# Performance work log

Measured on AMD Instinct MI355X. Metric: run time of the kernel, lower is better.

Reference implementation:

```python
import jax, jax.numpy as jnp
import numpy as np

B, S, D_IN, D_OUT, H = 4, 2048, 1024, 1024, 16
HD = D_OUT // H

def setup_inputs() -> dict:
    key = jax.random.key(0)
    ks = jax.random.split(key, 6)
    s = 1.0 / np.sqrt(D_IN)
    return {
        "x": jax.random.normal(ks[0], (B, S, D_IN), dtype=jnp.float32),
        "Wq": jax.random.uniform(ks[1], (D_IN, D_OUT), jnp.float32, -s, s),
        "Wk": jax.random.uniform(ks[2], (D_IN, D_OUT), jnp.float32, -s, s),
        "Wv": jax.random.uniform(ks[3], (D_IN, D_OUT), jnp.float32, -s, s),
        "Wo": jax.random.uniform(ks[4], (D_OUT, D_OUT), jnp.float32, -s, s),
        "bo": jax.random.uniform(ks[5], (D_OUT,), jnp.float32, -s, s),
    }

def reference(x, Wq, Wk, Wv, Wo, bo):
    b, n, _ = x.shape
    # project and split heads: [b, h, n, hd]
    q = (x @ Wq).reshape(b, n, H, HD).transpose(0, 2, 1, 3)
    k = (x @ Wk).reshape(b, n, H, HD).transpose(0, 2, 1, 3)
    v = (x @ Wv).reshape(b, n, H, HD).transpose(0, 2, 1, 3)
    scores = jnp.einsum("bhqd,bhkd->bhqk", q, k) / np.sqrt(HD).astype(np.float32)
    causal = jnp.tril(jnp.ones((n, n), dtype=bool))
    scores = jnp.where(causal, scores, -jnp.inf)
    attn = jax.nn.softmax(scores, axis=-1)  # dropout p=0.0 -> identity
    ctx = jnp.einsum("bhqk,bhkd->bhqd", attn, v)
    ctx = ctx.transpose(0, 2, 1, 3).reshape(b, n, D_OUT)
    return ctx @ Wo + bo
```

## Files before the change

kernel.cpp:

```cpp
#include <hip/hip_runtime.h>
#include <stdint.h>

#define B_   4
#define S_   2048
#define DI   1024
#define DOUT 1024
#define NHD  16
#define HD   64

typedef __attribute__((ext_vector_type(8))) short short8;
typedef __attribute__((ext_vector_type(4))) float f32x4;
typedef __attribute__((ext_vector_type(16))) float f32x16;

__device__ __forceinline__ unsigned short f32_bf16(float f) {
  union { float f; unsigned u; } v; v.f = f;
  unsigned r = v.u + 0x7FFFu + ((v.u >> 16) & 1u);
  return (unsigned short)(r >> 16);
}

__device__ __forceinline__ unsigned cvt_pk_bf16(float a, float b) {
  unsigned r;
  asm("v_cvt_pk_bf16_f32 %0, %1, %2" : "=v"(r) : "v"(a), "v"(b));
  return r;
}

__device__ __forceinline__ void pl32swap(unsigned &dst, unsigned &src) {
  asm("v_permlane32_swap_b32 %0, %1" : "+v"(dst), "+v"(src));
}

__device__ __forceinline__ float max3f(float a, float b, float c) {
  float d;
  asm("v_max3_f32 %0, %1, %2, %3" : "=v"(d) : "v"(a), "v"(b), "v"(c));
  return d;
}

__device__ __forceinline__ void gl_lds16(const void* g, void* s) {
  __builtin_amdgcn_global_load_lds(
      (const __attribute__((address_space(1))) unsigned int*)g,
      (__attribute__((address_space(3))) unsigned int*)s, 16, 0, 0);
}

#define EXP2(x) __builtin_amdgcn_exp2f(x)

__global__ __launch_bounds__(256) void cvt_kernel(const float* __restrict__ src,
                                                  unsigned short* __restrict__ dst, int n4) {
  int i = blockIdx.x * blockDim.x + threadIdx.x;
  if (i < n4) {
    float4 v = ((const float4*)src)[i];
    ushort4 o;
    o.x = f32_bf16(v.x); o.y = f32_bf16(v.y); o.z = f32_bf16(v.z); o.w = f32_bf16(v.w);
    ((ushort4*)dst)[i] = o;
  }
}

__global__ __launch_bounds__(256) void wtrans_kernel(const float* __restrict__ W,
                                                     unsigned short* __restrict__ Wt) {
  __shared__ __attribute__((aligned(16))) float tile[64][65];
  const int k0 = blockIdx.y * 64;
  const int n0 = blockIdx.x * 64;
  const int tid = threadIdx.x;
#pragma unroll
  for (int i = 0; i < 4; i++) {
    int c = tid + i * 256;
    int r = c >> 4;
    int cc = (c & 15) * 4;
    float4 v = *(const float4*)(W + (size_t)(k0 + r) * DOUT + n0 + cc);
    tile[r][cc] = v.x; tile[r][cc + 1] = v.y; tile[r][cc + 2] = v.z; tile[r][cc + 3] = v.w;
  }
  __syncthreads();
#pragma unroll
  for (int i = 0; i < 4; i++) {
    int c = tid + i * 256;
    int r = c >> 4;
    int cc = (c & 15) * 4;
    ushort4 o;
    o.x = f32_bf16(tile[cc + 0][r]);
    o.y = f32_bf16(tile[cc + 1][r]);
    o.z = f32_bf16(tile[cc + 2][r]);
    o.w = f32_bf16(tile[cc + 3][r]);
    *(ushort4*)(Wt + (size_t)(n0 + r) * DI + k0 + cc) = o;
  }
}

__global__ __launch_bounds__(256) void vtrans_kernel(const unsigned short* __restrict__ Vb,
                                                     unsigned short* __restrict__ Vt) {
  __shared__ __attribute__((aligned(16))) unsigned short tile[64][72];
  const int bh = blockIdx.y;
  const int s0 = blockIdx.x * 64;
  const int tid = threadIdx.x;
  const unsigned short* src = Vb + (size_t)bh * S_ * HD + (size_t)s0 * HD;
#pragma unroll
  for (int i = 0; i < 2; i++) {
    int c = tid + i * 256;
    int r = c >> 3;
    int cc = (c & 7) * 8;
    *(uint4*)(&tile[r][cc]) = *(const uint4*)(src + r * HD + cc);
  }
  __syncthreads();
  unsigned short* dst = Vt + (size_t)bh * HD * S_ + s0;
#pragma unroll
  for (int i = 0; i < 2; i++) {
    int c = tid + i * 256;
    int r = c >> 3;
    int cc = (c & 7) * 8;
    union { unsigned short u[8]; uint4 v; } t;
#pragma unroll
    for (int j = 0; j < 8; j++) t.u[j] = tile[cc + j][r];
    *(uint4*)(dst + (size_t)r * S_ + cc) = t.v;
  }
}

template <int MODE>
__global__ __launch_bounds__(256) void gemm_kernel(
    const unsigned short* __restrict__ A,
    const unsigned short* __restrict__ Bt,
    unsigned short* __restrict__ oQ,
    unsigned short* __restrict__ oK,
    unsigned short* __restrict__ oV,
    float* __restrict__ outF,
    const float* __restrict__ bias,
    int M, int N, int K) {
  __shared__ __attribute__((aligned(16))) unsigned short Asm_[128 * 32];
  __shared__ __attribute__((aligned(16))) unsigned short Bsm_[128 * 32];
  const int tid = threadIdx.x;
  const int lane = tid & 63;
  const int w = tid >> 6;
  const int wm = w >> 1, wn = w & 1;
  const int quad = lane >> 4, l16 = lane & 15;
  const int m0 = blockIdx.x * 128;
  const int n0 = blockIdx.y * 128;

  const int lr = lane >> 2;
  const int lc8 = (lane & 3) * 8;
  const unsigned short* gA0 = A + (size_t)(m0 + w * 32 + lr) * K + lc8;
  const unsigned short* gA1 = gA0 + (size_t)16 * K;
  const unsigned short* gB0 = Bt + (size_t)(n0 + w * 32 + lr) * K + lc8;
  const unsigned short* gB1 = gB0 + (size_t)16 * K;
  unsigned short* sA0 = Asm_ + (w * 2 + 0) * 512;
  unsigned short* sA1 = Asm_ + (w * 2 + 1) * 512;
  unsigned short* sB0 = Bsm_ + (w * 2 + 0) * 512;
  unsigned short* sB1 = Bsm_ + (w * 2 + 1) * 512;

  f32x4 acc[4][4] = {};

  for (int k0 = 0; k0 < K; k0 += 32) {
    __syncthreads();
    gl_lds16(gA0 + k0, sA0);
    gl_lds16(gA1 + k0, sA1);
    gl_lds16(gB0 + k0, sB0);
    gl_lds16(gB1 + k0, sB1);
    __syncthreads();
    short8 af[4], bfr[4];
#pragma unroll
    for (int mi = 0; mi < 4; mi++)
      af[mi] = *(const short8*)(Asm_ + (wm * 64 + mi * 16 + l16) * 32 + quad * 8);
#pragma unroll
    for (int ni = 0; ni < 4; ni++)
      bfr[ni] = *(const short8*)(Bsm_ + (wn * 64 + ni * 16 + l16) * 32 + quad * 8);
#pragma unroll
    for (int mi = 0; mi < 4; mi++)
#pragma unroll
      for (int ni = 0; ni < 4; ni++)
        acc[mi][ni] = __builtin_amdgcn_mfma_f32_16x16x32_bf16(af[mi], bfr[ni], acc[mi][ni], 0, 0, 0);
  }

  unsigned short* dst0 = nullptr;
  if (MODE == 0) {
    const int which = n0 >> 10;
    dst0 = which == 0 ? oQ : which == 1 ? oK : oV;
  }
#pragma unroll
  for (int mi = 0; mi < 4; mi++) {
#pragma unroll
    for (int ni = 0; ni < 4; ni++) {
      const int col = n0 + wn * 64 + ni * 16 + l16;
      float bv = (MODE == 1) ? bias[col] : 0.f;
#pragma unroll
      for (int r = 0; r < 4; r++) {
        const int row = m0 + wm * 64 + mi * 16 + quad * 4 + r;
        if (MODE == 0) {
          int b = row >> 11, s = row & 2047;
          int h = (col >> 6) & 15, hd = col & 63;
          dst0[(((size_t)(b * NHD + h)) * S_ + s) * HD + hd] = f32_bf16(acc[mi][ni][r]);
        } else {
          outF[(size_t)row * N + col] = acc[mi][ni][r] + bv;
        }
      }
    }
  }
}

__global__ __launch_bounds__(512, 4) void attn_kernel(
    const unsigned short* __restrict__ Q,
    const unsigned short* __restrict__ Kmat,
    const unsigned short* __restrict__ Vt,
    unsigned short* __restrict__ ctx) {
  __shared__ __attribute__((aligned(16))) unsigned short Ks[2][64 * 64];
  __shared__ __attribute__((aligned(16))) unsigned short Vs[2][64 * 64];
  __shared__ __attribute__((aligned(16))) unsigned short PsT[256 * 72];

  const int tid = threadIdx.x;
  const int lane = tid & 63;
  const int w = tid >> 6;
  const int l32 = lane & 31;
  const int h = lane >> 5;

  const int bh = blockIdx.x & 63;
  const int i4 = blockIdx.x >> 6;
  const int jj = (i4 < 4) ? 7 - i4 : i4 - 4;
  const int qc = jj * 8 + w;
  const int nt = (qc >> 1) + 1;
  const int ntmax = jj * 4 + 4;

  const unsigned short* Qh = Q + (size_t)bh * S_ * HD;
  const unsigned short* Kh = Kmat + (size_t)bh * S_ * HD;
  const unsigned short* Vh = Vt + (size_t)bh * HD * S_;

  const int qrow = qc * 32 + l32;

  short8 qf[4];
#pragma unroll
  for (int ks = 0; ks < 4; ks++)
    qf[ks] = *(const short8*)(Qh + (size_t)qrow * HD + ks * 16 + h * 8);

  const int sr = tid >> 3;
  const int sj = tid & 7;
  const int ssw = sr * 64 + ((sj ^ (sr & 7)) << 3);
  const unsigned short* gK = Kh + (size_t)sr * HD + sj * 8;
  const unsigned short* gV = Vh + (size_t)sr * S_ + sj * 8;
  const int swz = (l32 & 7);

  uint4 kreg = *(const uint4*)(gK);
  uint4 vreg = *(const uint4*)(gV);
  *(uint4*)(&Ks[0][ssw]) = kreg;
  *(uint4*)(&Vs[0][ssw]) = vreg;
  __syncthreads();

  f32x16 oacc[2] = {};
  float m_run = -__builtin_inff();
  float l_run = 0.f;
  unsigned short* myP = PsT + (size_t)(w * 32) * 72;
  const float scl = 0.18033688f;

  for (int kt = 0; kt < ntmax; kt++) {
    if (kt + 1 < ntmax) {
      kreg = *(const uint4*)(gK + (size_t)(kt + 1) * 64 * HD);
      vreg = *(const uint4*)(gV + (size_t)(kt + 1) * 64);
    }
    const unsigned short* Kb_ = Ks[kt & 1];
    const unsigned short* Vb_ = Vs[kt & 1];

    if (kt < nt) {
      const int k0 = kt * 64;
      f32x16 sacc[2] = {};
#pragma unroll
      for (int ks = 0; ks < 4; ks++)
#pragma unroll
        for (int mi = 0; mi < 2; mi++) {
          short8 kf = *(const short8*)(Kb_ + (mi * 32 + l32) * 64 + (((ks * 2 + h) ^ swz) << 3));
          sacc[mi] = __builtin_amdgcn_mfma_f32_32x32x16_bf16(kf, qf[ks], sacc[mi], 0, 0, 0);
        }

      if (kt == nt - 1) {
#pragma unroll
        for (int mi = 0; mi < 2; mi++)
#pragma unroll
          for (int e = 0; e < 16; e++) {
            int key = k0 + mi * 32 + (e & 3) + 8 * (e >> 2) + 4 * h;
            if (key > qrow) sacc[mi][e] = -__builtin_inff();
          }
      }
      float vmax = fmaxf(sacc[0][0], sacc[0][1]);
#pragma unroll
      for (int e = 2; e < 16; e += 2) vmax = max3f(vmax, sacc[0][e], sacc[0][e + 1]);
#pragma unroll
      for (int e = 0; e < 16; e += 2) vmax = max3f(vmax, sacc[1][e], sacc[1][e + 1]);
      vmax = fmaxf(vmax, __shfl_xor(vmax, 32));
      const float pm = vmax * scl;
      if (!__all(pm <= m_run + 8.f)) {
        const float mnew = fmaxf(m_run, pm);
        const float alpha = EXP2(m_run - mnew);
        m_run = mnew;
        l_run *= alpha;
#pragma unroll
        for (int mi = 0; mi < 2; mi++) oacc[mi] *= alpha;
      }

      float rs = 0.f;
#pragma unroll
      for (int mi = 0; mi < 2; mi++)
#pragma unroll
        for (int e = 0; e < 16; e++) {
          float p = EXP2(fmaf(sacc[mi][e], scl, -m_run));
          sacc[mi][e] = p;
          rs += p;
        }
      rs += __shfl_xor(rs, 32);
      l_run += rs;

      short8 pfr[4];
#pragma unroll
      for (int mi = 0; mi < 2; mi++) {
        unsigned w0 = cvt_pk_bf16(sacc[mi][0], sacc[mi][1]);
        unsigned w1 = cvt_pk_bf16(sacc[mi][2], sacc[mi][3]);
        unsigned w2 = cvt_pk_bf16(sacc[mi][4], sacc[mi][5]);
        unsigned w3 = cvt_pk_bf16(sacc[mi][6], sacc[mi][7]);
        pl32swap(w0, w2);
        pl32swap(w1, w3);
        union { unsigned u[4]; short8 s; } lo;
        lo.u[0] = w0; lo.u[1] = w1; lo.u[2] = w2; lo.u[3] = w3;
        pfr[2 * mi + 0] = lo.s;
        unsigned x0 = cvt_pk_bf16(sacc[mi][8], sacc[mi][9]);
        unsigned x1 = cvt_pk_bf16(sacc[mi][10], sacc[mi][11]);
        unsigned x2 = cvt_pk_bf16(sacc[mi][12], sacc[mi][13]);
        unsigned x3 = cvt_pk_bf16(sacc[mi][14], sacc[mi][15]);
        pl32swap(x0, x2);
        pl32swap(x1, x3);
        union { unsigned u[4]; short8 s; } hi;
        hi.u[0] = x0; hi.u[1] = x1; hi.u[2] = x2; hi.u[3] = x3;
        pfr[2 * mi + 1] = hi.s;
      }

#pragma unroll
      for (int ks2 = 0; ks2 < 4; ks2++) {
#pragma unroll
        for (int mi2 = 0; mi2 < 2; mi2++) {
          short8 vf = *(const short8*)(Vb_ + (mi2 * 32 + l32) * 64 + (((ks2 * 2 + h) ^ swz) << 3));
          oacc[mi2] = __builtin_amdgcn_mfma_f32_32x32x16_bf16(vf, pfr[ks2], oacc[mi2], 0, 0, 0);
        }
      }
    }

    if (kt + 1 < ntmax) {
      *(uint4*)(&Ks[(kt + 1) & 1][ssw]) = kreg;
      *(uint4*)(&Vs[(kt + 1) & 1][ssw]) = vreg;
    }
    __syncthreads();
  }

  const float inv = 1.f / l_run;
#pragma unroll
  for (int mi2 = 0; mi2 < 2; mi2++)
#pragma unroll
    for (int g = 0; g < 4; g++) {
      uint2 pk;
      pk.x = cvt_pk_bf16(oacc[mi2][4 * g + 0] * inv, oacc[mi2][4 * g + 1] * inv);
      pk.y = cvt_pk_bf16(oacc[mi2][4 * g + 2] * inv, oacc[mi2][4 * g + 3] * inv);
      *(uint2*)(myP + l32 * 72 + mi2 * 32 + g * 8 + h * 4) = pk;
    }
  const int b = bh >> 4, head = bh & 15;
#pragma unroll
  for (int p = 0; p < 4; p++) {
    int r = p * 8 + (lane >> 3);
    int c = (lane & 7) * 8;
    uint4 vv = *(const uint4*)(myP + r * 72 + c);
    *(uint4*)(ctx + ((size_t)(b * S_ + qc * 32 + r)) * DOUT + head * 64 + c) = vv;
  }
}

extern "C" void kernel_launch(void* const* d_in, const int* in_sizes, int n_in,
                              void* d_out, int out_size, void* d_ws, size_t ws_size,
                              hipStream_t stream) {
  const float* x  = (const float*)d_in[0];
  const float* Wq = (const float*)d_in[1];
  const float* Wk = (const float*)d_in[2];
  const float* Wv = (const float*)d_in[3];
  const float* Wo = (const float*)d_in[4];
  const float* bo = (const float*)d_in[5];
  float* out = (float*)d_out;
  char* ws = (char*)d_ws;

  const size_t MB = 1024 * 1024;
  unsigned short* Wqt = (unsigned short*)(ws + 0 * MB);
  unsigned short* Wkt = (unsigned short*)(ws + 2 * MB);
  unsigned short* Wvt = (unsigned short*)(ws + 4 * MB);
  unsigned short* Wot = (unsigned short*)(ws + 6 * MB);
  unsigned short* xb  = (unsigned short*)(ws + 8 * MB);
  unsigned short* Qb  = (unsigned short*)(ws + 24 * MB);
  unsigned short* Kb  = (unsigned short*)(ws + 40 * MB);
  unsigned short* Vb  = (unsigned short*)(ws + 56 * MB);
  unsigned short* Vtb = (unsigned short*)(ws + 72 * MB);
  unsigned short* ctxb = xb;

  cvt_kernel<<<8192, 256, 0, stream>>>(x, xb, 2097152);
  wtrans_kernel<<<dim3(16, 16), 256, 0, stream>>>(Wq, Wqt);
  wtrans_kernel<<<dim3(16, 16), 256, 0, stream>>>(Wk, Wkt);
  wtrans_kernel<<<dim3(16, 16), 256, 0, stream>>>(Wv, Wvt);
  wtrans_kernel<<<dim3(16, 16), 256, 0, stream>>>(Wo, Wot);
  gemm_kernel<0><<<dim3(64, 24), 256, 0, stream>>>(xb, Wqt, Qb, Kb, Vb, nullptr, nullptr,
                                                   8192, 3072, 1024);
  vtrans_kernel<<<dim3(32, 64), 256, 0, stream>>>(Vb, Vtb);
  attn_kernel<<<512, 512, 0, stream>>>(Qb, Kb, Vtb, ctxb);
  gemm_kernel<1><<<dim3(64, 8), 256, 0, stream>>>(ctxb, Wot, nullptr, nullptr, nullptr, out, bo,
                                                  8192, 1024, 1024);
}
```

Before: 271.4 us.

## Fuse V transpose into QKV GEMM epilogue and rebalance causal attention blocks

The QKV projection GEMM now writes the V tile transposed into LDS with an XOR swizzle and stores it directly in [b,h,d,s] layout, which removes the separate vtrans kernel and its extra global round trip. The attention kernel moves from 512-thread blocks to 256-thread blocks that each handle two query chunks in sequence, pairing a short causal row with its complementary long row so every block does similar work. This costs an LDS staging pass and extra syncs in the V epilogue, and each attention block now runs two serial key loops.

```diff
diff --git a/kernel.cpp b/kernel.cpp
--- a/kernel.cpp
+++ b/kernel.cpp
@@ -82,32 +82,8 @@
   }
 }
 
-__global__ __launch_bounds__(256) void vtrans_kernel(const unsigned short* __restrict__ Vb,
-                                                     unsigned short* __restrict__ Vt) {
-  __shared__ __attribute__((aligned(16))) unsigned short tile[64][72];
-  const int bh = blockIdx.y;
-  const int s0 = blockIdx.x * 64;
-  const int tid = threadIdx.x;
-  const unsigned short* src = Vb + (size_t)bh * S_ * HD + (size_t)s0 * HD;
-#pragma unroll
-  for (int i = 0; i < 2; i++) {
-    int c = tid + i * 256;
-    int r = c >> 3;
-    int cc = (c & 7) * 8;
-    *(uint4*)(&tile[r][cc]) = *(const uint4*)(src + r * HD + cc);
-  }
-  __syncthreads();
-  unsigned short* dst = Vt + (size_t)bh * HD * S_ + s0;
-#pragma unroll
-  for (int i = 0; i < 2; i++) {
-    int c = tid + i * 256;
-    int r = c >> 3;
-    int cc = (c & 7) * 8;
-    union { unsigned short u[8]; uint4 v; } t;
-#pragma unroll
-    for (int j = 0; j < 8; j++) t.u[j] = tile[cc + j][r];
-    *(uint4*)(dst + (size_t)r * S_ + cc) = t.v;
-  }
+__device__ __forceinline__ int cswz(int r, int c) {
+  return r * 128 + ((((c >> 3) ^ ((r >> 3) & 15)) << 3) | (c & 7));
 }
 
 template <int MODE>
@@ -120,8 +96,9 @@
     float* __restrict__ outF,
     const float* __restrict__ bias,
     int M, int N, int K) {
-  __shared__ __attribute__((aligned(16))) unsigned short Asm_[128 * 32];
-  __shared__ __attribute__((aligned(16))) unsigned short Bsm_[128 * 32];
+  __shared__ __attribute__((aligned(16))) unsigned short smem[MODE == 0 ? 16384 : 8192];
+  unsigned short* Asm_ = smem;
+  unsigned short* Bsm_ = smem + 4096;
   const int tid = threadIdx.x;
   const int lane = tid & 63;
   const int w = tid >> 6;
@@ -164,40 +141,72 @@
         acc[mi][ni] = __builtin_amdgcn_mfma_f32_16x16x32_bf16(af[mi], bfr[ni], acc[mi][ni], 0, 0, 0);
   }
 
-  unsigned short* dst0 = nullptr;
   if (MODE == 0) {
     const int which = n0 >> 10;
-    dst0 = which == 0 ? oQ : which == 1 ? oK : oV;
-  }
-#pragma unroll
-  for (int mi = 0; mi < 4; mi++) {
-#pragma unroll
-    for (int ni = 0; ni < 4; ni++) {
-      const int col = n0 + wn * 64 + ni * 16 + l16;
-      float bv = (MODE == 1) ? bias[col] : 0.f;
-#pragma unroll
-      for (int r = 0; r < 4; r++) {
-        const int row = m0 + wm * 64 + mi * 16 + quad * 4 + r;
-        if (MODE == 0) {
-          int b = row >> 11, s = row & 2047;
-          int h = (col >> 6) & 15, hd = col & 63;
-          dst0[(((size_t)(b * NHD + h)) * S_ + s) * HD + hd] = f32_bf16(acc[mi][ni][r]);
-        } else {
+    if (which == 2) {
+      __syncthreads();
+#pragma unroll
+      for (int mi = 0; mi < 4; mi++)
+#pragma unroll
+        for (int ni = 0; ni < 4; ni++)
+#pragma unroll
+          for (int r = 0; r < 4; r++)
+            smem[cswz(wm * 64 + mi * 16 + quad * 4 + r, wn * 64 + ni * 16 + l16)] =
+                f32_bf16(acc[mi][ni][r]);
+      __syncthreads();
+      const int b = m0 >> 11, sb = m0 & 2047;
+#pragma unroll
+      for (int i = 0; i < 8; i++) {
+        int c = tid + i * 256;
+        int cl = c >> 4;
+        int sc = (c & 15) * 8;
+        int col = n0 + cl;
+        int hh = (col >> 6) & 15, hd = col & 63;
+        union { unsigned short u[8]; uint4 v; } t;
+#pragma unroll
+        for (int j = 0; j < 8; j++) t.u[j] = smem[cswz(sc + j, cl)];
+        *(uint4*)(oV + (((size_t)(b * NHD + hh)) * HD + hd) * S_ + sb + sc) = t.v;
+      }
+    } else {
+      unsigned short* dst0 = which == 0 ? oQ : oK;
+#pragma unroll
+      for (int mi = 0; mi < 4; mi++)
+#pragma unroll
+        for (int ni = 0; ni < 4; ni++) {
+          const int col = n0 + wn * 64 + ni * 16 + l16;
+          const int hh = (col >> 6) & 15, hd = col & 63;
+#pragma unroll
+          for (int r = 0; r < 4; r++) {
+            const int row = m0 + wm * 64 + mi * 16 + quad * 4 + r;
+            int b = row >> 11, s = row & 2047;
+            dst0[(((size_t)(b * NHD + hh)) * S_ + s) * HD + hd] = f32_bf16(acc[mi][ni][r]);
+          }
+        }
+    }
+  } else {
+#pragma unroll
+    for (int mi = 0; mi < 4; mi++)
+#pragma unroll
+      for (int ni = 0; ni < 4; ni++) {
+        const int col = n0 + wn * 64 + ni * 16 + l16;
+        float bv = bias[col];
+#pragma unroll
+        for (int r = 0; r < 4; r++) {
+          const int row = m0 + wm * 64 + mi * 16 + quad * 4 + r;
           outF[(size_t)row * N + col] = acc[mi][ni][r] + bv;
         }
       }
-    }
-  }
-}
-
-__global__ __launch_bounds__(512, 4) void attn_kernel(
+  }
+}
+
+__global__ __launch_bounds__(256, 2) void attn_kernel(
     const unsigned short* __restrict__ Q,
     const unsigned short* __restrict__ Kmat,
     const unsigned short* __restrict__ Vt,
     unsigned short* __restrict__ ctx) {
   __shared__ __attribute__((aligned(16))) unsigned short Ks[2][64 * 64];
   __shared__ __attribute__((aligned(16))) unsigned short Vs[2][64 * 64];
-  __shared__ __attribute__((aligned(16))) unsigned short PsT[256 * 72];
+  __shared__ __attribute__((aligned(16))) unsigned short PsT[128 * 72];
 
   const int tid = threadIdx.x;
   const int lane = tid & 63;
@@ -206,155 +215,166 @@
   const int h = lane >> 5;
 
   const int bh = blockIdx.x & 63;
-  const int i4 = blockIdx.x >> 6;
-  const int jj = (i4 < 4) ? 7 - i4 : i4 - 4;
-  const int qc = jj * 8 + w;
-  const int nt = (qc >> 1) + 1;
-  const int ntmax = jj * 4 + 4;
+  const int jj = blockIdx.x >> 6;
 
   const unsigned short* Qh = Q + (size_t)bh * S_ * HD;
   const unsigned short* Kh = Kmat + (size_t)bh * S_ * HD;
   const unsigned short* Vh = Vt + (size_t)bh * HD * S_;
 
-  const int qrow = qc * 32 + l32;
-
-  short8 qf[4];
-#pragma unroll
-  for (int ks = 0; ks < 4; ks++)
-    qf[ks] = *(const short8*)(Qh + (size_t)qrow * HD + ks * 16 + h * 8);
-
-  const int sr = tid >> 3;
-  const int sj = tid & 7;
-  const int ssw = sr * 64 + ((sj ^ (sr & 7)) << 3);
-  const unsigned short* gK = Kh + (size_t)sr * HD + sj * 8;
-  const unsigned short* gV = Vh + (size_t)sr * S_ + sj * 8;
+  const int sr = tid >> 2;
+  const int jA = tid & 3, jB = jA + 4;
+  const int sswA = sr * 64 + ((jA ^ (sr & 7)) << 3);
+  const int sswB = sr * 64 + ((jB ^ (sr & 7)) << 3);
+  const unsigned short* gKA = Kh + (size_t)sr * HD + jA * 8;
+  const unsigned short* gKB = Kh + (size_t)sr * HD + jB * 8;
+  const unsigned short* gVA = Vh + (size_t)sr * S_ + jA * 8;
+  const unsigned short* gVB = Vh + (size_t)sr * S_ + jB * 8;
   const int swz = (l32 & 7);
 
-  uint4 kreg = *(const uint4*)(gK);
-  uint4 vreg = *(const uint4*)(gV);
-  *(uint4*)(&Ks[0][ssw]) = kreg;
-  *(uint4*)(&Vs[0][ssw]) = vreg;
-  __syncthreads();
-
-  f32x16 oacc[2] = {};
-  float m_run = -__builtin_inff();
-  float l_run = 0.f;
   unsigned short* myP = PsT + (size_t)(w * 32) * 72;
   const float scl = 0.18033688f;
-
-  for (int kt = 0; kt < ntmax; kt++) {
-    if (kt + 1 < ntmax) {
-      kreg = *(const uint4*)(gK + (size_t)(kt + 1) * 64 * HD);
-      vreg = *(const uint4*)(gV + (size_t)(kt + 1) * 64);
+  const int b = bh >> 4, head = bh & 15;
+
+  for (int ph = 0; ph < 2; ph++) {
+    const int qc = (ph == 0) ? (jj * 8 + w) : (63 - jj * 8 - w);
+    const int nt = (qc >> 1) + 1;
+    const int ntmax = (ph == 0) ? (jj * 4 + 2) : (32 - jj * 4);
+    const int qrow = qc * 32 + l32;
+
+    short8 qf[4];
+#pragma unroll
+    for (int ks = 0; ks < 4; ks++)
+      qf[ks] = *(const short8*)(Qh + (size_t)qrow * HD + ks * 16 + h * 8);
+
+    uint4 kregA = *(const uint4*)gKA, kregB = *(const uint4*)gKB;
+    uint4 vregA = *(const uint4*)gVA, vregB = *(const uint4*)gVB;
+    *(uint4*)(&Ks[0][sswA]) = kregA;
+    *(uint4*)(&Ks[0][sswB]) = kregB;
+    *(uint4*)(&Vs[0][sswA]) = vregA;
+    *(uint4*)(&Vs[0][sswB]) = vregB;
+    __syncthreads();
+
+    f32x16 oacc[2] = {};
+    float m_run = -__builtin_inff();
+    float l_run = 0.f;
+
+    for (int kt = 0; kt < ntmax; kt++) {
+      if (kt + 1 < ntmax) {
+        kregA = *(const uint4*)(gKA + (size_t)(kt + 1) * 64 * HD);
+        kregB = *(const uint4*)(gKB + (size_t)(kt + 1) * 64 * HD);
+        vregA = *(const uint4*)(gVA + (size_t)(kt + 1) * 64);
+        vregB = *(const uint4*)(gVB + (size_t)(kt + 1) * 64);
+      }
+      const unsigned short* Kb_ = Ks[kt & 1];
+      const unsigned short* Vb_ = Vs[kt & 1];
+
+      if (kt < nt) {
+        const int k0 = kt * 64;
+        f32x16 sacc[2] = {};
+#pragma unroll
+        for (int ks = 0; ks < 4; ks++)
+#pragma unroll
+          for (int mi = 0; mi < 2; mi++) {
+            short8 kf = *(const short8*)(Kb_ + (mi * 32 + l32) * 64 + (((ks * 2 + h) ^ swz) << 3));
+            sacc[mi] = __builtin_amdgcn_mfma_f32_32x32x16_bf16(kf, qf[ks], sacc[mi], 0, 0, 0);
+          }
+
+        if (kt == nt - 1) {
+#pragma unroll
+          for (int mi = 0; mi < 2; mi++)
+#pragma unroll
+            for (int e = 0; e < 16; e++) {
+              int key = k0 + mi * 32 + (e & 3) + 8 * (e >> 2) + 4 * h;
+              if (key > qrow) sacc[mi][e] = -__builtin_inff();
+            }
+        }
+        float vmax = fmaxf(sacc[0][0], sacc[0][1]);
+#pragma unroll
+        for (int e = 2; e < 16; e += 2) vmax = max3f(vmax, sacc[0][e], sacc[0][e + 1]);
+#pragma unroll
+        for (int e = 0; e < 16; e += 2) vmax = max3f(vmax, sacc[1][e], sacc[1][e + 1]);
+        vmax = fmaxf(vmax, __shfl_xor(vmax, 32));
+        const float pm = vmax * scl;
+        if (!__all(pm <= m_run + 8.f)) {
+          const float mnew = fmaxf(m_run, pm);
+          const float alpha = EXP2(m_run - mnew);
+          m_run = mnew;
+          l_run *= alpha;
+#pragma unroll
+          for (int mi = 0; mi < 2; mi++) oacc[mi] *= alpha;
+        }
+
+        float rs = 0.f;
+#pragma unroll
+        for (int mi = 0; mi < 2; mi++)
+#pragma unroll
+          for (int e = 0; e < 16; e++) {
+            float p = EXP2(fmaf(sacc[mi][e], scl, -m_run));
+            sacc[mi][e] = p;
+            rs += p;
+          }
+        rs += __shfl_xor(rs, 32);
+        l_run += rs;
+
+        short8 pfr[4];
+#pragma unroll
+        for (int mi = 0; mi < 2; mi++) {
+          unsigned w0 = cvt_pk_bf16(sacc[mi][0], sacc[mi][1]);
+          unsigned w1 = cvt_pk_bf16(sacc[mi][2], sacc[mi][3]);
+          unsigned w2 = cvt_pk_bf16(sacc[mi][4], sacc[mi][5]);
+          unsigned w3 = cvt_pk_bf16(sacc[mi][6], sacc[mi][7]);
+          pl32swap(w0, w2);
+          pl32swap(w1, w3);
+          union { unsigned u[4]; short8 s; } lo;
+          lo.u[0] = w0; lo.u[1] = w1; lo.u[2] = w2; lo.u[3] = w3;
+          pfr[2 * mi + 0] = lo.s;
+          unsigned x0 = cvt_pk_bf16(sacc[mi][8], sacc[mi][9]);
+          unsigned x1 = cvt_pk_bf16(sacc[mi][10], sacc[mi][11]);
+          unsigned x2 = cvt_pk_bf16(sacc[mi][12], sacc[mi][13]);
+          unsigned x3 = cvt_pk_bf16(sacc[mi][14], sacc[mi][15]);
+          pl32swap(x0, x2);
+          pl32swap(x1, x3);
+          union { unsigned u[4]; short8 s; } hi;
+          hi.u[0] = x0; hi.u[1] = x1; hi.u[2] = x2; hi.u[3] = x3;
+          pfr[2 * mi + 1] = hi.s;
+        }
+
+#pragma unroll
+        for (int ks2 = 0; ks2 < 4; ks2++) {
+#pragma unroll
+          for (int mi2 = 0; mi2 < 2; mi2++) {
+            short8 vf = *(const short8*)(Vb_ + (mi2 * 32 + l32) * 64 + (((ks2 * 2 + h) ^ swz) << 3));
+            oacc[mi2] = __builtin_amdgcn_mfma_f32_32x32x16_bf16(vf, pfr[ks2], oacc[mi2], 0, 0, 0);
+          }
+        }
+      }
+
+      if (kt + 1 < ntmax) {
+        *(uint4*)(&Ks[(kt + 1) & 1][sswA]) = kregA;
+        *(uint4*)(&Ks[(kt + 1) & 1][sswB]) = kregB;
+        *(uint4*)(&Vs[(kt + 1) & 1][sswA]) = vregA;
+        *(uint4*)(&Vs[(kt + 1) & 1][sswB]) = vregB;
+      }
+      __syncthreads();
     }
-    const unsigned short* Kb_ = Ks[kt & 1];
-    const unsigned short* Vb_ = Vs[kt & 1];
-
-    if (kt < nt) {
-      const int k0 = kt * 64;
-      f32x16 sacc[2] = {};
-#pragma unroll
-      for (int ks = 0; ks < 4; ks++)
-#pragma unroll
-        for (int mi = 0; mi < 2; mi++) {
-          short8 kf = *(const short8*)(Kb_ + (mi * 32 + l32) * 64 + (((ks * 2 + h) ^ swz) << 3));
-          sacc[mi] = __builtin_amdgcn_mfma_f32_32x32x16_bf16(kf, qf[ks], sacc[mi], 0, 0, 0);
-        }
-
-      if (kt == nt - 1) {
-#pragma unroll
-        for (int mi = 0; mi < 2; mi++)
-#pragma unroll
-          for (int e = 0; e < 16; e++) {
-            int key = k0 + mi * 32 + (e & 3) + 8 * (e >> 2) + 4 * h;
-            if (key > qrow) sacc[mi][e] = -__builtin_inff();
-          }
-      }
-      float vmax = fmaxf(sacc[0][0], sacc[0][1]);
-#pragma unroll
-      for (int e = 2; e < 16; e += 2) vmax = max3f(vmax, sacc[0][e], sacc[0][e + 1]);
-#pragma unroll
-      for (int e = 0; e < 16; e += 2) vmax = max3f(vmax, sacc[1][e], sacc[1][e + 1]);
-      vmax = fmaxf(vmax, __shfl_xor(vmax, 32));
-      const float pm = vmax * scl;
-      if (!__all(pm <= m_run + 8.f)) {
-        const float mnew = fmaxf(m_run, pm);
-        const float alpha = EXP2(m_run - mnew);
-        m_run = mnew;
-        l_run *= alpha;
-#pragma unroll
-        for (int mi = 0; mi < 2; mi++) oacc[mi] *= alpha;
-      }
-
-      float rs = 0.f;
-#pragma unroll
-      for (int mi = 0; mi < 2; mi++)
-#pragma unroll
-        for (int e = 0; e < 16; e++) {
-          float p = EXP2(fmaf(sacc[mi][e], scl, -m_run));
-          sacc[mi][e] = p;
-          rs += p;
-        }
-      rs += __shfl_xor(rs, 32);
-      l_run += rs;
-
-      short8 pfr[4];
-#pragma unroll
-      for (int mi = 0; mi < 2; mi++) {
-        unsigned w0 = cvt_pk_bf16(sacc[mi][0], sacc[mi][1]);
-        unsigned w1 = cvt_pk_bf16(sacc[mi][2], sacc[mi][3]);
-        unsigned w2 = cvt_pk_bf16(sacc[mi][4], sacc[mi][5]);
-        unsigned w3 = cvt_pk_bf16(sacc[mi][6], sacc[mi][7]);
-        pl32swap(w0, w2);
-        pl32swap(w1, w3);
-        union { unsigned u[4]; short8 s; } lo;
-        lo.u[0] = w0; lo.u[1] = w1; lo.u[2] = w2; lo.u[3] = w3;
-        pfr[2 * mi + 0] = lo.s;
-        unsigned x0 = cvt_pk_bf16(sacc[mi][8], sacc[mi][9]);
-        unsigned x1 = cvt_pk_bf16(sacc[mi][10], sacc[mi][11]);
-        unsigned x2 = cvt_pk_bf16(sacc[mi][12], sacc[mi][13]);
-        unsigned x3 = cvt_pk_bf16(sacc[mi][14], sacc[mi][15]);
-        pl32swap(x0, x2);
-        pl32swap(x1, x3);
-        union { unsigned u[4]; short8 s; } hi;
-        hi.u[0] = x0; hi.u[1] = x1; hi.u[2] = x2; hi.u[3] = x3;
-        pfr[2 * mi + 1] = hi.s;
-      }
-
-#pragma unroll
-      for (int ks2 = 0; ks2 < 4; ks2++) {
-#pragma unroll
-        for (int mi2 = 0; mi2 < 2; mi2++) {
-          short8 vf = *(const short8*)(Vb_ + (mi2 * 32 + l32) * 64 + (((ks2 * 2 + h) ^ swz) << 3));
-          oacc[mi2] = __builtin_amdgcn_mfma_f32_32x32x16_bf16(vf, pfr[ks2], oacc[mi2], 0, 0, 0);
-        }
-      }
+
+    const float inv = 1.f / l_run;
+#pragma unroll
+    for (int mi2 = 0; mi2 < 2; mi2++)
+#pragma unroll
+      for (int g = 0; g < 4; g++) {
+        uint2 pk;
+        pk.x = cvt_pk_bf16(oacc[mi2][4 * g + 0] * inv, oacc[mi2][4 * g + 1] * inv);
+        pk.y = cvt_pk_bf16(oacc[mi2][4 * g + 2] * inv, oacc[mi2][4 * g + 3] * inv);
+        *(uint2*)(myP + l32 * 72 + mi2 * 32 + g * 8 + h * 4) = pk;
+      }
+#pragma unroll
+    for (int p = 0; p < 4; p++) {
+      int r = p * 8 + (lane >> 3);
+      int c = (lane & 7) * 8;
+      uint4 vv = *(const uint4*)(myP + r * 72 + c);
+      *(uint4*)(ctx + ((size_t)(b * S_ + qc * 32 + r)) * DOUT + head * 64 + c) = vv;
     }
-
-    if (kt + 1 < ntmax) {
-      *(uint4*)(&Ks[(kt + 1) & 1][ssw]) = kreg;
-      *(uint4*)(&Vs[(kt + 1) & 1][ssw]) = vreg;
-    }
-    __syncthreads();
-  }
-
-  const float inv = 1.f / l_run;
-#pragma unroll
-  for (int mi2 = 0; mi2 < 2; mi2++)
-#pragma unroll
-    for (int g = 0; g < 4; g++) {
-      uint2 pk;
-      pk.x = cvt_pk_bf16(oacc[mi2][4 * g + 0] * inv, oacc[mi2][4 * g + 1] * inv);
-      pk.y = cvt_pk_bf16(oacc[mi2][4 * g + 2] * inv, oacc[mi2][4 * g + 3] * inv);
-      *(uint2*)(myP + l32 * 72 + mi2 * 32 + g * 8 + h * 4) = pk;
-    }
-  const int b = bh >> 4, head = bh & 15;
-#pragma unroll
-  for (int p = 0; p < 4; p++) {
-    int r = p * 8 + (lane >> 3);
-    int c = (lane & 7) * 8;
-    uint4 vv = *(const uint4*)(myP + r * 72 + c);
-    *(uint4*)(ctx + ((size_t)(b * S_ + qc * 32 + r)) * DOUT + head * 64 + c) = vv;
   }
 }
 
@@ -378,7 +398,6 @@
   unsigned short* xb  = (unsigned short*)(ws + 8 * MB);
   unsigned short* Qb  = (unsigned short*)(ws + 24 * MB);
   unsigned short* Kb  = (unsigned short*)(ws + 40 * MB);
-  unsigned short* Vb  = (unsigned short*)(ws + 56 * MB);
   unsigned short* Vtb = (unsigned short*)(ws + 72 * MB);
   unsigned short* ctxb = xb;
 
@@ -387,10 +406,9 @@
   wtrans_kernel<<<dim3(16, 16), 256, 0, stream>>>(Wk, Wkt);
   wtrans_kernel<<<dim3(16, 16), 256, 0, stream>>>(Wv, Wvt);
   wtrans_kernel<<<dim3(16, 16), 256, 0, stream>>>(Wo, Wot);
-  gemm_kernel<0><<<dim3(64, 24), 256, 0, stream>>>(xb, Wqt, Qb, Kb, Vb, nullptr, nullptr,
+  gemm_kernel<0><<<dim3(64, 24), 256, 0, stream>>>(xb, Wqt, Qb, Kb, Vtb, nullptr, nullptr,
                                                    8192, 3072, 1024);
-  vtrans_kernel<<<dim3(32, 64), 256, 0, stream>>>(Vb, Vtb);
-  attn_kernel<<<512, 512, 0, stream>>>(Qb, Kb, Vtb, ctxb);
+  attn_kernel<<<512, 256, 0, stream>>>(Qb, Kb, Vtb, ctxb);
   gemm_kernel<1><<<dim3(64, 8), 256, 0, stream>>>(ctxb, Wot, nullptr, nullptr, nullptr, out, bo,
                                                   8192, 1024, 1024);
 }
```

Result: faster. 255.3 us (-5.9%).
